# Kernel optimization log

Measured on AMD Instinct MI355X. Metric: run time of the kernel, lower is better.

Reference implementation:

```python
import jax, jax.numpy as jnp
import numpy as np
from jax.ops import segment_sum

N_NODES = 500_000
N_EDGES = 16_000_000


def gcn_conv(x, W, b, src, dst, n_nodes):
    """PyG GCNConv: linear transform, add self-loops, sym deg norm, scatter-add."""
    xw = x @ W  # [N, out]
    # degree including self-loop (edge weight 1 each)
    deg = segment_sum(jnp.ones((src.shape[0],), xw.dtype), dst, num_segments=n_nodes) + 1.0
    dinv = jax.lax.rsqrt(deg)  # deg^{-1/2}, deg >= 1 so safe
    norm = dinv[src] * dinv[dst]  # [E]
    msg = xw[src] * norm[:, None]  # [E, out]
    agg = segment_sum(msg, dst, num_segments=n_nodes)
    # self-loop contribution: norm_ii = dinv_i^2
    agg = agg + xw * (dinv * dinv)[:, None]
    return agg + b


def setup_inputs() -> dict:
    key = jax.random.key(0)
    ks = jax.random.split(key, 8)
    x = jax.random.normal(ks[0], (N_NODES, 2), dtype=jnp.float32)
    edge_index = jax.random.randint(ks[1], (2, N_EDGES), 0, N_NODES, dtype=jnp.int64)
    def glorot(k, fan_in, fan_out):
        s = jnp.sqrt(6.0 / (fan_in + fan_out))
        return jax.random.uniform(k, (fan_in, fan_out), jnp.float32, -s, s)
    return {
        "x": x,
        "edge_index": edge_index,
        "W1": glorot(ks[2], 2, 4), "b1": jnp.zeros((4,), jnp.float32),
        "W2": glorot(ks[3], 4, 4), "b2": jnp.zeros((4,), jnp.float32),
        "W3": glorot(ks[4], 4, 2), "b3": jnp.zeros((2,), jnp.float32),
    }


def reference(x, edge_index, W1, b1, W2, b2, W3, b3):
    src, dst = edge_index[0], edge_index[1]
    n = x.shape[0]
    h = jnp.tanh(gcn_conv(x, W1, b1, src, dst, n))
    h = jnp.tanh(gcn_conv(h, W2, b2, src, dst, n))
    h = gcn_conv(h, W3, b3, src, dst, n)
    return h
```

## Files before the change

kernel.cpp:

```cpp
#include <hip/hip_runtime.h>
#include <hip/hip_fp16.h>


#define TPB 256
#define T_TILE 16384
#define FBB 10
#define FB_MAX 512
#define CAP_F 34048
#define EB_CAP 34048

__global__ void initcur(int* __restrict__ cur, int FB) {
    int t = threadIdx.x;
    if (t < FB) cur[t] = t * CAP_F;
}

__global__ void __launch_bounds__(512)
scatter1(const int* __restrict__ dst, const int* __restrict__ src,
         int* __restrict__ cur, unsigned* __restrict__ pk1, int E, int FB) {
    __shared__ unsigned lpk[T_TILE];
    __shared__ int lhist[FB_MAX];
    __shared__ int lexcl[FB_MAX];
    __shared__ int lcur[FB_MAX];
    __shared__ int lbase[FB_MAX];
    int blk = blockIdx.x, tid = threadIdx.x;
    lhist[tid] = 0;
    __syncthreads();
    int base = blk * T_TILE;
    #pragma unroll 8
    for (int it = 0; it < T_TILE / 512; ++it) {
        int e = base + it * 512 + tid;
        if (e < E) atomicAdd(&lhist[((unsigned)dst[e]) >> FBB], 1);
    }
    __syncthreads();
    int hv = lhist[tid];
    lexcl[tid] = hv;
    __syncthreads();
    for (int off = 1; off < FB_MAX; off <<= 1) {
        int a = (tid >= off) ? lexcl[tid - off] : 0;
        __syncthreads();
        lexcl[tid] += a;
        __syncthreads();
    }
    lexcl[tid] -= hv;
    lcur[tid] = lexcl[tid];
    if (tid < FB && hv > 0) lbase[tid] = atomicAdd(&cur[tid], hv);
    __syncthreads();
    #pragma unroll 8
    for (int it = 0; it < T_TILE / 512; ++it) {
        int e = base + it * 512 + tid;
        if (e < E) {
            unsigned d = (unsigned)dst[e];
            unsigned s = (unsigned)src[e];
            int pos = atomicAdd(&lcur[d >> FBB], 1);
            lpk[pos] = (d & 1023u) | (s << FBB);
        }
    }
    __syncthreads();
    int w = tid >> 6, lane = tid & 63;
    for (int fb = w; fb < FB; fb += 8) {
        int cntb = lhist[fb];
        if (cntb == 0) continue;
        int lo = lexcl[fb], gb = lbase[fb];
        for (int t2 = lane; t2 < cntb; t2 += 64)
            pk1[gb + t2] = lpk[lo + t2];
    }
}

__global__ void bases_fix(const int* __restrict__ cur, int* __restrict__ csrbase,
                          int* __restrict__ rowptr, int FB, int N, int E) {
    __shared__ int lds[FB_MAX];
    int t = threadIdx.x;
    int c = (t < FB) ? (cur[t] - t * CAP_F) : 0;
    lds[t] = c;
    __syncthreads();
    for (int off = 1; off < FB_MAX; off <<= 1) {
        int a = (t >= off) ? lds[t - off] : 0;
        __syncthreads();
        lds[t] += a;
        __syncthreads();
    }
    if (t < FB) csrbase[t] = lds[t] - c;
    if (t == 0) { csrbase[FB] = E; rowptr[N] = E; }
}

__global__ void __launch_bounds__(1024)
buildfine(const unsigned* __restrict__ pk1, const int* __restrict__ csrbase,
          const float* __restrict__ x, int* __restrict__ rowptr,
          float* __restrict__ dinv, unsigned* __restrict__ z1h,
          unsigned* __restrict__ csr, int N) {
    __shared__ int cnt[1024];
    __shared__ int tmp[1024];
    __shared__ int cur[1024];
    __shared__ unsigned eb[EB_CAP];
    int fb = blockIdx.x, tid = threadIdx.x;
    int cb = csrbase[fb];
    int n = csrbase[fb + 1] - cb;
    size_t pbase = (size_t)fb * CAP_F;
    cnt[tid] = 0;
    __syncthreads();
    int k0 = 0;
    for (; k0 + 8192 <= n; k0 += 8192) {
        unsigned p[8];
        #pragma unroll
        for (int u = 0; u < 8; ++u) p[u] = pk1[pbase + k0 + tid + u * 1024];
        #pragma unroll
        for (int u = 0; u < 8; ++u) atomicAdd(&cnt[p[u] & 1023u], 1);
    }
    for (int k = k0 + tid; k < n; k += 1024)
        atomicAdd(&cnt[pk1[pbase + k] & 1023u], 1);
    __syncthreads();
    int c = cnt[tid];
    tmp[tid] = c;
    __syncthreads();
    for (int o = 1; o < 1024; o <<= 1) {
        int a = (tid >= o) ? tmp[tid - o] : 0;
        __syncthreads();
        tmp[tid] += a;
        __syncthreads();
    }
    int excl = tmp[tid] - c;
    int i = (fb << FBB) + tid;
    if (i < N) {
        rowptr[i] = cb + excl;
        float di = rsqrtf((float)c + 1.0f);
        dinv[i] = di;
        float2 xv = ((const float2*)x)[i];
        __half2 hz = __floats2half2_rn(xv.x * di, xv.y * di);
        z1h[i] = *(unsigned*)&hz;
    }
    cur[tid] = excl;
    __syncthreads();
    if (n <= EB_CAP) {
        k0 = 0;
        for (; k0 + 8192 <= n; k0 += 8192) {
            unsigned p[8];
            #pragma unroll
            for (int u = 0; u < 8; ++u) p[u] = pk1[pbase + k0 + tid + u * 1024];
            #pragma unroll
            for (int u = 0; u < 8; ++u) {
                int pos = atomicAdd(&cur[p[u] & 1023u], 1);
                eb[pos] = p[u] >> FBB;
            }
        }
        for (int k = k0 + tid; k < n; k += 1024) {
            unsigned p = pk1[pbase + k];
            int pos = atomicAdd(&cur[p & 1023u], 1);
            eb[pos] = p >> FBB;
        }
        __syncthreads();
        for (int k = tid; k < n; k += 1024) csr[cb + k] = eb[k];
    } else {
        for (int k = tid; k < n; k += 1024) {
            unsigned p = pk1[pbase + k];
            int pos = atomicAdd(&cur[p & 1023u], 1);
            csr[cb + pos] = p >> FBB;
        }
    }
}


__global__ void gcn1(const int* __restrict__ rowptr, const unsigned* __restrict__ csr,
                     const unsigned* __restrict__ z1h, const float* __restrict__ W1,
                     const float* __restrict__ b1, const float* __restrict__ dinv,
                     uint2* __restrict__ z2h, int N) {
    int i = blockIdx.x * blockDim.x + threadIdx.x;
    if (i >= N) return;
    int r0 = rowptr[i], r1 = rowptr[i + 1];
    float a0, a1;
    {
        unsigned zr = z1h[i];
        float2 zi = __half22float2(*(__half2*)&zr);
        a0 = zi.x; a1 = zi.y;
    }
    int k = r0;
    for (; k + 16 <= r1; k += 16) {
        unsigned j[16];
        #pragma unroll
        for (int u = 0; u < 16; ++u) j[u] = __builtin_nontemporal_load(&csr[k + u]);
        unsigned raw[16];
        #pragma unroll
        for (int u = 0; u < 16; ++u) raw[u] = z1h[j[u]];
        #pragma unroll
        for (int u = 0; u < 16; ++u) {
            float2 v = __half22float2(*(__half2*)&raw[u]);
            a0 += v.x; a1 += v.y;
        }
    }
    for (; k < r1; ++k) {
        unsigned zr = z1h[csr[k]];
        float2 zv = __half22float2(*(__half2*)&zr);
        a0 += zv.x; a1 += zv.y;
    }
    float di = dinv[i];
    float g0 = di * a0, g1 = di * a1;
    float o0 = di * tanhf(fmaf(g0, W1[0], fmaf(g1, W1[4], b1[0])));
    float o1 = di * tanhf(fmaf(g0, W1[1], fmaf(g1, W1[5], b1[1])));
    float o2 = di * tanhf(fmaf(g0, W1[2], fmaf(g1, W1[6], b1[2])));
    float o3 = di * tanhf(fmaf(g0, W1[3], fmaf(g1, W1[7], b1[3])));
    __half2 ha = __floats2half2_rn(o0, o1);
    __half2 hb = __floats2half2_rn(o2, o3);
    uint2 packed;
    packed.x = *(unsigned*)&ha;
    packed.y = *(unsigned*)&hb;
    z2h[i] = packed;
}

__global__ void gcn2(const int* __restrict__ rowptr, const unsigned* __restrict__ csr,
                     const uint2* __restrict__ z2h, const float* __restrict__ W2,
                     const float* __restrict__ b2, const float* __restrict__ W3,
                     const float* __restrict__ dinv, unsigned* __restrict__ z3h, int N) {
    int i = blockIdx.x * blockDim.x + threadIdx.x;
    if (i >= N) return;
    int r0 = rowptr[i], r1 = rowptr[i + 1];
    float a0, a1, a2, a3;
    {
        uint2 raw = z2h[i];
        float2 f01 = __half22float2(*(__half2*)&raw.x);
        float2 f23 = __half22float2(*(__half2*)&raw.y);
        a0 = f01.x; a1 = f01.y; a2 = f23.x; a3 = f23.y;
    }
    int k = r0;
    for (; k + 8 <= r1; k += 8) {
        unsigned j[8];
        #pragma unroll
        for (int u = 0; u < 8; ++u) j[u] = __builtin_nontemporal_load(&csr[k + u]);
        uint2 raw[8];
        #pragma unroll
        for (int u = 0; u < 8; ++u) raw[u] = z2h[j[u]];
        #pragma unroll
        for (int u = 0; u < 8; ++u) {
            float2 f01 = __half22float2(*(__half2*)&raw[u].x);
            float2 f23 = __half22float2(*(__half2*)&raw[u].y);
            a0 += f01.x; a1 += f01.y; a2 += f23.x; a3 += f23.y;
        }
    }
    for (; k < r1; ++k) {
        uint2 raw = z2h[csr[k]];
        float2 f01 = __half22float2(*(__half2*)&raw.x);
        float2 f23 = __half22float2(*(__half2*)&raw.y);
        a0 += f01.x; a1 += f01.y; a2 += f23.x; a3 += f23.y;
    }
    float di = dinv[i];
    float g0 = di * a0, g1 = di * a1, g2 = di * a2, g3 = di * a3;
    float h[4];
    #pragma unroll
    for (int c = 0; c < 4; ++c)
        h[c] = tanhf(b2[c] + g0 * W2[c] + g1 * W2[4 + c] + g2 * W2[8 + c] + g3 * W2[12 + c]);
    float v0 = h[0] * W3[0] + h[1] * W3[2] + h[2] * W3[4] + h[3] * W3[6];
    float v1 = h[0] * W3[1] + h[1] * W3[3] + h[2] * W3[5] + h[3] * W3[7];
    __half2 hz = __floats2half2_rn(v0 * di, v1 * di);
    z3h[i] = *(unsigned*)&hz;
}

__global__ void gcn3(const int* __restrict__ rowptr, const unsigned* __restrict__ csr,
                     const unsigned* __restrict__ z3h, const float* __restrict__ b3,
                     const float* __restrict__ dinv, float* __restrict__ out, int N) {
    int i = blockIdx.x * blockDim.x + threadIdx.x;
    if (i >= N) return;
    int r0 = rowptr[i], r1 = rowptr[i + 1];
    float a0, a1;
    {
        unsigned zr = z3h[i];
        float2 zi = __half22float2(*(__half2*)&zr);
        a0 = zi.x; a1 = zi.y;
    }
    int k = r0;
    for (; k + 16 <= r1; k += 16) {
        unsigned j[16];
        #pragma unroll
        for (int u = 0; u < 16; ++u) j[u] = __builtin_nontemporal_load(&csr[k + u]);
        unsigned raw[16];
        #pragma unroll
        for (int u = 0; u < 16; ++u) raw[u] = z3h[j[u]];
        #pragma unroll
        for (int u = 0; u < 16; ++u) {
            float2 v = __half22float2(*(__half2*)&raw[u]);
            a0 += v.x; a1 += v.y;
        }
    }
    for (; k < r1; ++k) {
        unsigned zr = z3h[csr[k]];
        float2 zv = __half22float2(*(__half2*)&zr);
        a0 += zv.x; a1 += zv.y;
    }
    float di = dinv[i];
    ((float2*)out)[i] = make_float2(fmaf(di, a0, b3[0]), fmaf(di, a1, b3[1]));
}

extern "C" void kernel_launch(void* const* d_in, const int* in_sizes, int n_in,
                              void* d_out, int out_size, void* d_ws, size_t ws_size,
                              hipStream_t stream) {
    const float* x  = (const float*)d_in[0];
    const int*   ei = (const int*)d_in[1];
    const float* W1 = (const float*)d_in[2];
    const float* b1 = (const float*)d_in[3];
    const float* W2 = (const float*)d_in[4];
    const float* b2 = (const float*)d_in[5];
    const float* W3 = (const float*)d_in[6];
    const float* b3 = (const float*)d_in[7];
    float* out = (float*)d_out;

    const int N = in_sizes[0] / 2;
    const int E = in_sizes[1] / 2;
    const int* src = ei;
    const int* dst = ei + E;

    const int FB  = (N + (1 << FBB) - 1) >> FBB;
    const int ntB = (E + T_TILE - 1) / T_TILE;

    auto align = [](size_t o) { return (o + 255) & ~(size_t)255; };
    char* wbase = (char*)d_ws;
    size_t off = 0;
    float*    dinv    = (float*)(wbase + off);    off = align(off + (size_t)N * 4);
    unsigned* z1h     = (unsigned*)(wbase + off); off = align(off + (size_t)N * 4);
    uint2*    z2h     = (uint2*)(wbase + off);    off = align(off + (size_t)N * 8);
    unsigned* z3h     = (unsigned*)(wbase + off); off = align(off + (size_t)N * 4);
    int*      rowptr  = (int*)(wbase + off);      off = align(off + (size_t)(N + 1) * 4);
    int*      cur     = (int*)(wbase + off);      off = align(off + (size_t)FB_MAX * 4);
    int*      csrbase = (int*)(wbase + off);      off = align(off + (size_t)(FB_MAX + 1) * 4);
    unsigned* pk1     = (unsigned*)(wbase + off); off = align(off + (size_t)FB * CAP_F * 4);
    unsigned* csr     = (unsigned*)(wbase + off); off = align(off + (size_t)E * 4);

    dim3 gN((N + TPB - 1) / TPB);
    initcur<<<dim3(1), dim3(512), 0, stream>>>(cur, FB);
    scatter1<<<dim3(ntB), dim3(512), 0, stream>>>(dst, src, cur, pk1, E, FB);
    bases_fix<<<dim3(1), dim3(512), 0, stream>>>(cur, csrbase, rowptr, FB, N, E);
    buildfine<<<dim3(FB), dim3(1024), 0, stream>>>(pk1, csrbase, x, rowptr, dinv,
                                                   z1h, csr, N);
    gcn1<<<gN, dim3(TPB), 0, stream>>>(rowptr, csr, z1h, W1, b1, dinv, z2h, N);
    gcn2<<<gN, dim3(TPB), 0, stream>>>(rowptr, csr, z2h, W2, b2, W3, dinv, z3h, N);
    gcn3<<<gN, dim3(TPB), 0, stream>>>(rowptr, csr, z3h, b3, dinv, out, N);
}
```

Measured before the change: 715.4 us.

## Drop CSR build; aggregate per dst bucket with LDS atomics from packed edges

Replaces the fine CSR construction (prefix scan, local sort, CSR write) with a degree-only pass. Each layer now walks the coarse dst-bucketed packed edge array per 1024-node block and accumulates neighbour features with shared-memory float atomics. This removes one full pass that writes the CSR and the rowptr indirection. In exchange, every layer pays LDS atomics per edge, only FB (~489) blocks run, and the summation order becomes nondeterministic.

New measurement: 988.5 us. +38.2%, slower.

```diff
diff --git a/kernel.cpp b/kernel.cpp
--- a/kernel.cpp
+++ b/kernel.cpp
@@ -7,7 +7,6 @@
 #define FBB 10
 #define FB_MAX 512
 #define CAP_F 34048
-#define EB_CAP 34048
 
 __global__ void initcur(int* __restrict__ cur, int FB) {
     int t = threadIdx.x;
@@ -66,225 +65,261 @@
     }
 }
 
-__global__ void bases_fix(const int* __restrict__ cur, int* __restrict__ csrbase,
-                          int* __restrict__ rowptr, int FB, int N, int E) {
-    __shared__ int lds[FB_MAX];
-    int t = threadIdx.x;
-    int c = (t < FB) ? (cur[t] - t * CAP_F) : 0;
-    lds[t] = c;
-    __syncthreads();
-    for (int off = 1; off < FB_MAX; off <<= 1) {
-        int a = (t >= off) ? lds[t - off] : 0;
-        __syncthreads();
-        lds[t] += a;
-        __syncthreads();
-    }
-    if (t < FB) csrbase[t] = lds[t] - c;
-    if (t == 0) { csrbase[FB] = E; rowptr[N] = E; }
-}
-
 __global__ void __launch_bounds__(1024)
-buildfine(const unsigned* __restrict__ pk1, const int* __restrict__ csrbase,
-          const float* __restrict__ x, int* __restrict__ rowptr,
-          float* __restrict__ dinv, unsigned* __restrict__ z1h,
-          unsigned* __restrict__ csr, int N) {
-    __shared__ int cnt[1024];
-    __shared__ int tmp[1024];
-    __shared__ int cur[1024];
-    __shared__ unsigned eb[EB_CAP];
+builddeg(const unsigned* __restrict__ pk1, const int* __restrict__ cur,
+         const float* __restrict__ x, float* __restrict__ dinv,
+         unsigned* __restrict__ z1h, int N) {
+    __shared__ int deg[1024];
     int fb = blockIdx.x, tid = threadIdx.x;
-    int cb = csrbase[fb];
-    int n = csrbase[fb + 1] - cb;
+    deg[tid] = 0;
+    __syncthreads();
     size_t pbase = (size_t)fb * CAP_F;
-    cnt[tid] = 0;
-    __syncthreads();
+    int n = cur[fb] - (int)(fb * CAP_F);
     int k0 = 0;
     for (; k0 + 8192 <= n; k0 += 8192) {
         unsigned p[8];
         #pragma unroll
-        for (int u = 0; u < 8; ++u) p[u] = pk1[pbase + k0 + tid + u * 1024];
-        #pragma unroll
-        for (int u = 0; u < 8; ++u) atomicAdd(&cnt[p[u] & 1023u], 1);
+        for (int u = 0; u < 8; ++u)
+            p[u] = __builtin_nontemporal_load(&pk1[pbase + k0 + tid + u * 1024]);
+        #pragma unroll
+        for (int u = 0; u < 8; ++u) atomicAdd(&deg[p[u] & 1023u], 1);
     }
     for (int k = k0 + tid; k < n; k += 1024)
-        atomicAdd(&cnt[pk1[pbase + k] & 1023u], 1);
-    __syncthreads();
-    int c = cnt[tid];
-    tmp[tid] = c;
-    __syncthreads();
-    for (int o = 1; o < 1024; o <<= 1) {
-        int a = (tid >= o) ? tmp[tid - o] : 0;
-        __syncthreads();
-        tmp[tid] += a;
-        __syncthreads();
-    }
-    int excl = tmp[tid] - c;
+        atomicAdd(&deg[__builtin_nontemporal_load(&pk1[pbase + k]) & 1023u], 1);
+    __syncthreads();
     int i = (fb << FBB) + tid;
     if (i < N) {
-        rowptr[i] = cb + excl;
-        float di = rsqrtf((float)c + 1.0f);
+        float di = rsqrtf((float)deg[tid] + 1.0f);
         dinv[i] = di;
         float2 xv = ((const float2*)x)[i];
         __half2 hz = __floats2half2_rn(xv.x * di, xv.y * di);
         z1h[i] = *(unsigned*)&hz;
     }
-    cur[tid] = excl;
-    __syncthreads();
-    if (n <= EB_CAP) {
-        k0 = 0;
-        for (; k0 + 8192 <= n; k0 += 8192) {
-            unsigned p[8];
-            #pragma unroll
-            for (int u = 0; u < 8; ++u) p[u] = pk1[pbase + k0 + tid + u * 1024];
-            #pragma unroll
-            for (int u = 0; u < 8; ++u) {
-                int pos = atomicAdd(&cur[p[u] & 1023u], 1);
-                eb[pos] = p[u] >> FBB;
-            }
-        }
-        for (int k = k0 + tid; k < n; k += 1024) {
-            unsigned p = pk1[pbase + k];
-            int pos = atomicAdd(&cur[p & 1023u], 1);
-            eb[pos] = p >> FBB;
-        }
-        __syncthreads();
-        for (int k = tid; k < n; k += 1024) csr[cb + k] = eb[k];
-    } else {
-        for (int k = tid; k < n; k += 1024) {
-            unsigned p = pk1[pbase + k];
-            int pos = atomicAdd(&cur[p & 1023u], 1);
-            csr[cb + pos] = p >> FBB;
-        }
-    }
-}
-
-
-__global__ void gcn1(const int* __restrict__ rowptr, const unsigned* __restrict__ csr,
-                     const unsigned* __restrict__ z1h, const float* __restrict__ W1,
-                     const float* __restrict__ b1, const float* __restrict__ dinv,
-                     uint2* __restrict__ z2h, int N) {
-    int i = blockIdx.x * blockDim.x + threadIdx.x;
-    if (i >= N) return;
-    int r0 = rowptr[i], r1 = rowptr[i + 1];
-    float a0, a1;
-    {
+}
+
+
+__global__ void __launch_bounds__(1024)
+glayer1(const unsigned* __restrict__ pk1, const int* __restrict__ cur,
+        const unsigned* __restrict__ z1h, const float* __restrict__ dinv,
+        const float* __restrict__ W1, const float* __restrict__ b1,
+        uint2* __restrict__ z2h, int N) {
+    __shared__ float acc[2048];
+    int fb = blockIdx.x, tid = threadIdx.x;
+    acc[tid] = 0.f; acc[tid + 1024] = 0.f;
+    __syncthreads();
+    size_t pbase = (size_t)fb * CAP_F;
+    int n = cur[fb] - (int)(fb * CAP_F);
+    int k0 = 0;
+    for (; k0 + 16384 <= n; k0 += 16384) {
+        unsigned p[16];
+        #pragma unroll
+        for (int u = 0; u < 16; ++u)
+            p[u] = __builtin_nontemporal_load(&pk1[pbase + k0 + tid + u * 1024]);
+        unsigned raw[16];
+        #pragma unroll
+        for (int u = 0; u < 16; ++u) raw[u] = z1h[p[u] >> FBB];
+        #pragma unroll
+        for (int u = 0; u < 16; ++u) {
+            float2 v = __half22float2(*(__half2*)&raw[u]);
+            unsigned d = (p[u] & 1023u) << 1;
+            atomicAdd(&acc[d], v.x);
+            atomicAdd(&acc[d + 1], v.y);
+        }
+    }
+    for (; k0 + 4096 <= n; k0 += 4096) {
+        unsigned p[4];
+        #pragma unroll
+        for (int u = 0; u < 4; ++u)
+            p[u] = __builtin_nontemporal_load(&pk1[pbase + k0 + tid + u * 1024]);
+        unsigned raw[4];
+        #pragma unroll
+        for (int u = 0; u < 4; ++u) raw[u] = z1h[p[u] >> FBB];
+        #pragma unroll
+        for (int u = 0; u < 4; ++u) {
+            float2 v = __half22float2(*(__half2*)&raw[u]);
+            unsigned d = (p[u] & 1023u) << 1;
+            atomicAdd(&acc[d], v.x);
+            atomicAdd(&acc[d + 1], v.y);
+        }
+    }
+    for (int k = k0 + tid; k < n; k += 1024) {
+        unsigned p = __builtin_nontemporal_load(&pk1[pbase + k]);
+        unsigned zr = z1h[p >> FBB];
+        float2 v = __half22float2(*(__half2*)&zr);
+        unsigned d = (p & 1023u) << 1;
+        atomicAdd(&acc[d], v.x);
+        atomicAdd(&acc[d + 1], v.y);
+    }
+    __syncthreads();
+    int i = (fb << FBB) + tid;
+    if (i < N) {
         unsigned zr = z1h[i];
         float2 zi = __half22float2(*(__half2*)&zr);
-        a0 = zi.x; a1 = zi.y;
-    }
-    int k = r0;
-    for (; k + 16 <= r1; k += 16) {
-        unsigned j[16];
-        #pragma unroll
-        for (int u = 0; u < 16; ++u) j[u] = __builtin_nontemporal_load(&csr[k + u]);
+        float di = dinv[i];
+        float g0 = di * (acc[tid * 2] + zi.x);
+        float g1 = di * (acc[tid * 2 + 1] + zi.y);
+        float o0 = di * tanhf(fmaf(g0, W1[0], fmaf(g1, W1[4], b1[0])));
+        float o1 = di * tanhf(fmaf(g0, W1[1], fmaf(g1, W1[5], b1[1])));
+        float o2 = di * tanhf(fmaf(g0, W1[2], fmaf(g1, W1[6], b1[2])));
+        float o3 = di * tanhf(fmaf(g0, W1[3], fmaf(g1, W1[7], b1[3])));
+        __half2 ha = __floats2half2_rn(o0, o1);
+        __half2 hb = __floats2half2_rn(o2, o3);
+        uint2 packed;
+        packed.x = *(unsigned*)&ha;
+        packed.y = *(unsigned*)&hb;
+        z2h[i] = packed;
+    }
+}
+
+__global__ void __launch_bounds__(1024)
+glayer2(const unsigned* __restrict__ pk1, const int* __restrict__ cur,
+        const unsigned long long* __restrict__ z2h, const float* __restrict__ dinv,
+        const float* __restrict__ W2, const float* __restrict__ b2,
+        const float* __restrict__ W3, unsigned* __restrict__ z3h, int N) {
+    __shared__ float acc[4096];
+    int fb = blockIdx.x, tid = threadIdx.x;
+    #pragma unroll
+    for (int u = 0; u < 4; ++u) acc[tid + u * 1024] = 0.f;
+    __syncthreads();
+    size_t pbase = (size_t)fb * CAP_F;
+    int n = cur[fb] - (int)(fb * CAP_F);
+    int k0 = 0;
+    for (; k0 + 8192 <= n; k0 += 8192) {
+        unsigned p[8];
+        #pragma unroll
+        for (int u = 0; u < 8; ++u)
+            p[u] = __builtin_nontemporal_load(&pk1[pbase + k0 + tid + u * 1024]);
+        unsigned long long raw[8];
+        #pragma unroll
+        for (int u = 0; u < 8; ++u) raw[u] = z2h[p[u] >> FBB];
+        #pragma unroll
+        for (int u = 0; u < 8; ++u) {
+            unsigned lo = (unsigned)raw[u], hi = (unsigned)(raw[u] >> 32);
+            float2 f01 = __half22float2(*(__half2*)&lo);
+            float2 f23 = __half22float2(*(__half2*)&hi);
+            unsigned d = (p[u] & 1023u) << 2;
+            atomicAdd(&acc[d], f01.x);
+            atomicAdd(&acc[d + 1], f01.y);
+            atomicAdd(&acc[d + 2], f23.x);
+            atomicAdd(&acc[d + 3], f23.y);
+        }
+    }
+    for (; k0 + 4096 <= n; k0 += 4096) {
+        unsigned p[4];
+        #pragma unroll
+        for (int u = 0; u < 4; ++u)
+            p[u] = __builtin_nontemporal_load(&pk1[pbase + k0 + tid + u * 1024]);
+        unsigned long long raw[4];
+        #pragma unroll
+        for (int u = 0; u < 4; ++u) raw[u] = z2h[p[u] >> FBB];
+        #pragma unroll
+        for (int u = 0; u < 4; ++u) {
+            unsigned lo = (unsigned)raw[u], hi = (unsigned)(raw[u] >> 32);
+            float2 f01 = __half22float2(*(__half2*)&lo);
+            float2 f23 = __half22float2(*(__half2*)&hi);
+            unsigned d = (p[u] & 1023u) << 2;
+            atomicAdd(&acc[d], f01.x);
+            atomicAdd(&acc[d + 1], f01.y);
+            atomicAdd(&acc[d + 2], f23.x);
+            atomicAdd(&acc[d + 3], f23.y);
+        }
+    }
+    for (int k = k0 + tid; k < n; k += 1024) {
+        unsigned p = __builtin_nontemporal_load(&pk1[pbase + k]);
+        unsigned long long zr = z2h[p >> FBB];
+        unsigned lo = (unsigned)zr, hi = (unsigned)(zr >> 32);
+        float2 f01 = __half22float2(*(__half2*)&lo);
+        float2 f23 = __half22float2(*(__half2*)&hi);
+        unsigned d = (p & 1023u) << 2;
+        atomicAdd(&acc[d], f01.x);
+        atomicAdd(&acc[d + 1], f01.y);
+        atomicAdd(&acc[d + 2], f23.x);
+        atomicAdd(&acc[d + 3], f23.y);
+    }
+    __syncthreads();
+    int i = (fb << FBB) + tid;
+    if (i < N) {
+        unsigned long long zr = z2h[i];
+        unsigned lo = (unsigned)zr, hi = (unsigned)(zr >> 32);
+        float2 f01 = __half22float2(*(__half2*)&lo);
+        float2 f23 = __half22float2(*(__half2*)&hi);
+        float di = dinv[i];
+        float g0 = di * (acc[tid * 4] + f01.x);
+        float g1 = di * (acc[tid * 4 + 1] + f01.y);
+        float g2 = di * (acc[tid * 4 + 2] + f23.x);
+        float g3 = di * (acc[tid * 4 + 3] + f23.y);
+        float h[4];
+        #pragma unroll
+        for (int c = 0; c < 4; ++c)
+            h[c] = tanhf(b2[c] + g0 * W2[c] + g1 * W2[4 + c] + g2 * W2[8 + c] + g3 * W2[12 + c]);
+        float v0 = h[0] * W3[0] + h[1] * W3[2] + h[2] * W3[4] + h[3] * W3[6];
+        float v1 = h[0] * W3[1] + h[1] * W3[3] + h[2] * W3[5] + h[3] * W3[7];
+        __half2 hz = __floats2half2_rn(v0 * di, v1 * di);
+        z3h[i] = *(unsigned*)&hz;
+    }
+}
+
+__global__ void __launch_bounds__(1024)
+glayer3(const unsigned* __restrict__ pk1, const int* __restrict__ cur,
+        const unsigned* __restrict__ z3h, const float* __restrict__ dinv,
+        const float* __restrict__ b3, float* __restrict__ out, int N) {
+    __shared__ float acc[2048];
+    int fb = blockIdx.x, tid = threadIdx.x;
+    acc[tid] = 0.f; acc[tid + 1024] = 0.f;
+    __syncthreads();
+    size_t pbase = (size_t)fb * CAP_F;
+    int n = cur[fb] - (int)(fb * CAP_F);
+    int k0 = 0;
+    for (; k0 + 16384 <= n; k0 += 16384) {
+        unsigned p[16];
+        #pragma unroll
+        for (int u = 0; u < 16; ++u)
+            p[u] = __builtin_nontemporal_load(&pk1[pbase + k0 + tid + u * 1024]);
         unsigned raw[16];
         #pragma unroll
-        for (int u = 0; u < 16; ++u) raw[u] = z1h[j[u]];
+        for (int u = 0; u < 16; ++u) raw[u] = z3h[p[u] >> FBB];
         #pragma unroll
         for (int u = 0; u < 16; ++u) {
             float2 v = __half22float2(*(__half2*)&raw[u]);
-            a0 += v.x; a1 += v.y;
-        }
-    }
-    for (; k < r1; ++k) {
-        unsigned zr = z1h[csr[k]];
-        float2 zv = __half22float2(*(__half2*)&zr);
-        a0 += zv.x; a1 += zv.y;
-    }
-    float di = dinv[i];
-    float g0 = di * a0, g1 = di * a1;
-    float o0 = di * tanhf(fmaf(g0, W1[0], fmaf(g1, W1[4], b1[0])));
-    float o1 = di * tanhf(fmaf(g0, W1[1], fmaf(g1, W1[5], b1[1])));
-    float o2 = di * tanhf(fmaf(g0, W1[2], fmaf(g1, W1[6], b1[2])));
-    float o3 = di * tanhf(fmaf(g0, W1[3], fmaf(g1, W1[7], b1[3])));
-    __half2 ha = __floats2half2_rn(o0, o1);
-    __half2 hb = __floats2half2_rn(o2, o3);
-    uint2 packed;
-    packed.x = *(unsigned*)&ha;
-    packed.y = *(unsigned*)&hb;
-    z2h[i] = packed;
-}
-
-__global__ void gcn2(const int* __restrict__ rowptr, const unsigned* __restrict__ csr,
-                     const uint2* __restrict__ z2h, const float* __restrict__ W2,
-                     const float* __restrict__ b2, const float* __restrict__ W3,
-                     const float* __restrict__ dinv, unsigned* __restrict__ z3h, int N) {
-    int i = blockIdx.x * blockDim.x + threadIdx.x;
-    if (i >= N) return;
-    int r0 = rowptr[i], r1 = rowptr[i + 1];
-    float a0, a1, a2, a3;
-    {
-        uint2 raw = z2h[i];
-        float2 f01 = __half22float2(*(__half2*)&raw.x);
-        float2 f23 = __half22float2(*(__half2*)&raw.y);
-        a0 = f01.x; a1 = f01.y; a2 = f23.x; a3 = f23.y;
-    }
-    int k = r0;
-    for (; k + 8 <= r1; k += 8) {
-        unsigned j[8];
-        #pragma unroll
-        for (int u = 0; u < 8; ++u) j[u] = __builtin_nontemporal_load(&csr[k + u]);
-        uint2 raw[8];
-        #pragma unroll
-        for (int u = 0; u < 8; ++u) raw[u] = z2h[j[u]];
-        #pragma unroll
-        for (int u = 0; u < 8; ++u) {
-            float2 f01 = __half22float2(*(__half2*)&raw[u].x);
-            float2 f23 = __half22float2(*(__half2*)&raw[u].y);
-            a0 += f01.x; a1 += f01.y; a2 += f23.x; a3 += f23.y;
-        }
-    }
-    for (; k < r1; ++k) {
-        uint2 raw = z2h[csr[k]];
-        float2 f01 = __half22float2(*(__half2*)&raw.x);
-        float2 f23 = __half22float2(*(__half2*)&raw.y);
-        a0 += f01.x; a1 += f01.y; a2 += f23.x; a3 += f23.y;
-    }
-    float di = dinv[i];
-    float g0 = di * a0, g1 = di * a1, g2 = di * a2, g3 = di * a3;
-    float h[4];
-    #pragma unroll
-    for (int c = 0; c < 4; ++c)
-        h[c] = tanhf(b2[c] + g0 * W2[c] + g1 * W2[4 + c] + g2 * W2[8 + c] + g3 * W2[12 + c]);
-    float v0 = h[0] * W3[0] + h[1] * W3[2] + h[2] * W3[4] + h[3] * W3[6];
-    float v1 = h[0] * W3[1] + h[1] * W3[3] + h[2] * W3[5] + h[3] * W3[7];
-    __half2 hz = __floats2half2_rn(v0 * di, v1 * di);
-    z3h[i] = *(unsigned*)&hz;
-}
-
-__global__ void gcn3(const int* __restrict__ rowptr, const unsigned* __restrict__ csr,
-                     const unsigned* __restrict__ z3h, const float* __restrict__ b3,
-                     const float* __restrict__ dinv, float* __restrict__ out, int N) {
-    int i = blockIdx.x * blockDim.x + threadIdx.x;
-    if (i >= N) return;
-    int r0 = rowptr[i], r1 = rowptr[i + 1];
-    float a0, a1;
-    {
+            unsigned d = (p[u] & 1023u) << 1;
+            atomicAdd(&acc[d], v.x);
+            atomicAdd(&acc[d + 1], v.y);
+        }
+    }
+    for (; k0 + 4096 <= n; k0 += 4096) {
+        unsigned p[4];
+        #pragma unroll
+        for (int u = 0; u < 4; ++u)
+            p[u] = __builtin_nontemporal_load(&pk1[pbase + k0 + tid + u * 1024]);
+        unsigned raw[4];
+        #pragma unroll
+        for (int u = 0; u < 4; ++u) raw[u] = z3h[p[u] >> FBB];
+        #pragma unroll
+        for (int u = 0; u < 4; ++u) {
+            float2 v = __half22float2(*(__half2*)&raw[u]);
+            unsigned d = (p[u] & 1023u) << 1;
+            atomicAdd(&acc[d], v.x);
+            atomicAdd(&acc[d + 1], v.y);
+        }
+    }
+    for (int k = k0 + tid; k < n; k += 1024) {
+        unsigned p = __builtin_nontemporal_load(&pk1[pbase + k]);
+        unsigned zr = z3h[p >> FBB];
+        float2 v = __half22float2(*(__half2*)&zr);
+        unsigned d = (p & 1023u) << 1;
+        atomicAdd(&acc[d], v.x);
+        atomicAdd(&acc[d + 1], v.y);
+    }
+    __syncthreads();
+    int i = (fb << FBB) + tid;
+    if (i < N) {
         unsigned zr = z3h[i];
         float2 zi = __half22float2(*(__half2*)&zr);
-        a0 = zi.x; a1 = zi.y;
-    }
-    int k = r0;
-    for (; k + 16 <= r1; k += 16) {
-        unsigned j[16];
-        #pragma unroll
-        for (int u = 0; u < 16; ++u) j[u] = __builtin_nontemporal_load(&csr[k + u]);
-        unsigned raw[16];
-        #pragma unroll
-        for (int u = 0; u < 16; ++u) raw[u] = z3h[j[u]];
-        #pragma unroll
-        for (int u = 0; u < 16; ++u) {
-            float2 v = __half22float2(*(__half2*)&raw[u]);
-            a0 += v.x; a1 += v.y;
-        }
-    }
-    for (; k < r1; ++k) {
-        unsigned zr = z3h[csr[k]];
-        float2 zv = __half22float2(*(__half2*)&zr);
-        a0 += zv.x; a1 += zv.y;
-    }
-    float di = dinv[i];
-    ((float2*)out)[i] = make_float2(fmaf(di, a0, b3[0]), fmaf(di, a1, b3[1]));
+        float di = dinv[i];
+        float a0 = acc[tid * 2] + zi.x;
+        float a1 = acc[tid * 2 + 1] + zi.y;
+        ((float2*)out)[i] = make_float2(fmaf(di, a0, b3[0]), fmaf(di, a1, b3[1]));
+    }
 }
 
 extern "C" void kernel_launch(void* const* d_in, const int* in_sizes, int n_in,
@@ -311,23 +346,20 @@
     auto align = [](size_t o) { return (o + 255) & ~(size_t)255; };
     char* wbase = (char*)d_ws;
     size_t off = 0;
-    float*    dinv    = (float*)(wbase + off);    off = align(off + (size_t)N * 4);
-    unsigned* z1h     = (unsigned*)(wbase + off); off = align(off + (size_t)N * 4);
-    uint2*    z2h     = (uint2*)(wbase + off);    off = align(off + (size_t)N * 8);
-    unsigned* z3h     = (unsigned*)(wbase + off); off = align(off + (size_t)N * 4);
-    int*      rowptr  = (int*)(wbase + off);      off = align(off + (size_t)(N + 1) * 4);
-    int*      cur     = (int*)(wbase + off);      off = align(off + (size_t)FB_MAX * 4);
-    int*      csrbase = (int*)(wbase + off);      off = align(off + (size_t)(FB_MAX + 1) * 4);
-    unsigned* pk1     = (unsigned*)(wbase + off); off = align(off + (size_t)FB * CAP_F * 4);
-    unsigned* csr     = (unsigned*)(wbase + off); off = align(off + (size_t)E * 4);
-
-    dim3 gN((N + TPB - 1) / TPB);
+    float*    dinv = (float*)(wbase + off);    off = align(off + (size_t)N * 4);
+    unsigned* z1h  = (unsigned*)(wbase + off); off = align(off + (size_t)N * 4);
+    unsigned long long* z2h = (unsigned long long*)(wbase + off);
+    off = align(off + (size_t)N * 8);
+    unsigned* z3h  = (unsigned*)(wbase + off); off = align(off + (size_t)N * 4);
+    int*      cur  = (int*)(wbase + off);      off = align(off + (size_t)FB_MAX * 4);
+    unsigned* pk1  = (unsigned*)(wbase + off); off = align(off + (size_t)FB * CAP_F * 4);
+
     initcur<<<dim3(1), dim3(512), 0, stream>>>(cur, FB);
     scatter1<<<dim3(ntB), dim3(512), 0, stream>>>(dst, src, cur, pk1, E, FB);
-    bases_fix<<<dim3(1), dim3(512), 0, stream>>>(cur, csrbase, rowptr, FB, N, E);
-    buildfine<<<dim3(FB), dim3(1024), 0, stream>>>(pk1, csrbase, x, rowptr, dinv,
-                                                   z1h, csr, N);
-    gcn1<<<gN, dim3(TPB), 0, stream>>>(rowptr, csr, z1h, W1, b1, dinv, z2h, N);
-    gcn2<<<gN, dim3(TPB), 0, stream>>>(rowptr, csr, z2h, W2, b2, W3, dinv, z3h, N);
-    gcn3<<<gN, dim3(TPB), 0, stream>>>(rowptr, csr, z3h, b3, dinv, out, N);
-}
+    builddeg<<<dim3(FB), dim3(1024), 0, stream>>>(pk1, cur, x, dinv, z1h, N);
+    glayer1<<<dim3(FB), dim3(1024), 0, stream>>>(pk1, cur, z1h, dinv, W1, b1,
+                                                 (uint2*)z2h, N);
+    glayer2<<<dim3(FB), dim3(1024), 0, stream>>>(pk1, cur, z2h, dinv, W2, b2, W3,
+                                                 z3h, N);
+    glayer3<<<dim3(FB), dim3(1024), 0, stream>>>(pk1, cur, z3h, dinv, b3, out, N);
+}
```

## Sort nodes by degree within blocks to balance per-thread gather work

Applied to the files above, without the earlier changes.

Builds a per-1024-node-block permutation that groups nodes by in-degree (capped at 127) using a small shared histogram and scan in buildfine. The three GCN layer kernels then process nodes in permuted order, so threads in a wavefront have similar edge counts and less divergence in the gather loop. gcn2's gather unroll also grows from 8 to 16. The cost is an extra perm read per thread, less coalesced rowptr/dinv/output accesses, and more register pressure in gcn2.

Measured after the change: 850.4 us. 18.9% more time.

```diff
diff --git a/kernel.cpp b/kernel.cpp
--- a/kernel.cpp
+++ b/kernel.cpp
@@ -87,16 +87,19 @@
 buildfine(const unsigned* __restrict__ pk1, const int* __restrict__ csrbase,
           const float* __restrict__ x, int* __restrict__ rowptr,
           float* __restrict__ dinv, unsigned* __restrict__ z1h,
-          unsigned* __restrict__ csr, int N) {
+          unsigned* __restrict__ csr, int* __restrict__ perm, int N) {
     __shared__ int cnt[1024];
     __shared__ int tmp[1024];
     __shared__ int cur[1024];
     __shared__ unsigned eb[EB_CAP];
+    __shared__ int dh[128];
+    __shared__ int dcur[128];
     int fb = blockIdx.x, tid = threadIdx.x;
     int cb = csrbase[fb];
     int n = csrbase[fb + 1] - cb;
     size_t pbase = (size_t)fb * CAP_F;
     cnt[tid] = 0;
+    if (tid < 128) dh[tid] = 0;
     __syncthreads();
     int k0 = 0;
     for (; k0 + 8192 <= n; k0 += 8192) {
@@ -129,6 +132,23 @@
         z1h[i] = *(unsigned*)&hz;
     }
     cur[tid] = excl;
+    int dcap = (c < 127) ? c : 127;
+    if (i < N) atomicAdd(&dh[dcap], 1);
+    __syncthreads();
+    if (tid < 128) dcur[tid] = dh[tid];
+    __syncthreads();
+    for (int o = 1; o < 128; o <<= 1) {
+        int a = (tid < 128 && tid >= o) ? dcur[tid - o] : 0;
+        __syncthreads();
+        if (tid < 128) dcur[tid] += a;
+        __syncthreads();
+    }
+    if (tid < 128) dcur[tid] -= dh[tid];
+    __syncthreads();
+    if (i < N) {
+        int r = atomicAdd(&dcur[dcap], 1);
+        perm[(fb << FBB) + r] = i;
+    }
     __syncthreads();
     if (n <= EB_CAP) {
         k0 = 0;
@@ -160,11 +180,13 @@
 
 
 __global__ void gcn1(const int* __restrict__ rowptr, const unsigned* __restrict__ csr,
+                     const int* __restrict__ perm,
                      const unsigned* __restrict__ z1h, const float* __restrict__ W1,
                      const float* __restrict__ b1, const float* __restrict__ dinv,
                      uint2* __restrict__ z2h, int N) {
-    int i = blockIdx.x * blockDim.x + threadIdx.x;
-    if (i >= N) return;
+    int ii = blockIdx.x * blockDim.x + threadIdx.x;
+    if (ii >= N) return;
+    int i = perm[ii];
     int r0 = rowptr[i], r1 = rowptr[i + 1];
     float a0, a1;
     {
@@ -206,11 +228,13 @@
 }
 
 __global__ void gcn2(const int* __restrict__ rowptr, const unsigned* __restrict__ csr,
+                     const int* __restrict__ perm,
                      const uint2* __restrict__ z2h, const float* __restrict__ W2,
                      const float* __restrict__ b2, const float* __restrict__ W3,
                      const float* __restrict__ dinv, unsigned* __restrict__ z3h, int N) {
-    int i = blockIdx.x * blockDim.x + threadIdx.x;
-    if (i >= N) return;
+    int ii = blockIdx.x * blockDim.x + threadIdx.x;
+    if (ii >= N) return;
+    int i = perm[ii];
     int r0 = rowptr[i], r1 = rowptr[i + 1];
     float a0, a1, a2, a3;
     {
@@ -220,15 +244,15 @@
         a0 = f01.x; a1 = f01.y; a2 = f23.x; a3 = f23.y;
     }
     int k = r0;
-    for (; k + 8 <= r1; k += 8) {
-        unsigned j[8];
-        #pragma unroll
-        for (int u = 0; u < 8; ++u) j[u] = __builtin_nontemporal_load(&csr[k + u]);
-        uint2 raw[8];
-        #pragma unroll
-        for (int u = 0; u < 8; ++u) raw[u] = z2h[j[u]];
-        #pragma unroll
-        for (int u = 0; u < 8; ++u) {
+    for (; k + 16 <= r1; k += 16) {
+        unsigned j[16];
+        #pragma unroll
+        for (int u = 0; u < 16; ++u) j[u] = __builtin_nontemporal_load(&csr[k + u]);
+        uint2 raw[16];
+        #pragma unroll
+        for (int u = 0; u < 16; ++u) raw[u] = z2h[j[u]];
+        #pragma unroll
+        for (int u = 0; u < 16; ++u) {
             float2 f01 = __half22float2(*(__half2*)&raw[u].x);
             float2 f23 = __half22float2(*(__half2*)&raw[u].y);
             a0 += f01.x; a1 += f01.y; a2 += f23.x; a3 += f23.y;
@@ -253,10 +277,12 @@
 }
 
 __global__ void gcn3(const int* __restrict__ rowptr, const unsigned* __restrict__ csr,
+                     const int* __restrict__ perm,
                      const unsigned* __restrict__ z3h, const float* __restrict__ b3,
                      const float* __restrict__ dinv, float* __restrict__ out, int N) {
-    int i = blockIdx.x * blockDim.x + threadIdx.x;
-    if (i >= N) return;
+    int ii = blockIdx.x * blockDim.x + threadIdx.x;
+    if (ii >= N) return;
+    int i = perm[ii];
     int r0 = rowptr[i], r1 = rowptr[i + 1];
     float a0, a1;
     {
@@ -316,6 +342,7 @@
     uint2*    z2h     = (uint2*)(wbase + off);    off = align(off + (size_t)N * 8);
     unsigned* z3h     = (unsigned*)(wbase + off); off = align(off + (size_t)N * 4);
     int*      rowptr  = (int*)(wbase + off);      off = align(off + (size_t)(N + 1) * 4);
+    int*      perm    = (int*)(wbase + off);      off = align(off + (size_t)N * 4);
     int*      cur     = (int*)(wbase + off);      off = align(off + (size_t)FB_MAX * 4);
     int*      csrbase = (int*)(wbase + off);      off = align(off + (size_t)(FB_MAX + 1) * 4);
     unsigned* pk1     = (unsigned*)(wbase + off); off = align(off + (size_t)FB * CAP_F * 4);
@@ -326,8 +353,8 @@
     scatter1<<<dim3(ntB), dim3(512), 0, stream>>>(dst, src, cur, pk1, E, FB);
     bases_fix<<<dim3(1), dim3(512), 0, stream>>>(cur, csrbase, rowptr, FB, N, E);
     buildfine<<<dim3(FB), dim3(1024), 0, stream>>>(pk1, csrbase, x, rowptr, dinv,
-                                                   z1h, csr, N);
-    gcn1<<<gN, dim3(TPB), 0, stream>>>(rowptr, csr, z1h, W1, b1, dinv, z2h, N);
-    gcn2<<<gN, dim3(TPB), 0, stream>>>(rowptr, csr, z2h, W2, b2, W3, dinv, z3h, N);
-    gcn3<<<gN, dim3(TPB), 0, stream>>>(rowptr, csr, z3h, b3, dinv, out, N);
-}
+                                                   z1h, csr, perm, N);
+    gcn1<<<gN, dim3(TPB), 0, stream>>>(rowptr, csr, perm, z1h, W1, b1, dinv, z2h, N);
+    gcn2<<<gN, dim3(TPB), 0, stream>>>(rowptr, csr, perm, z2h, W2, b2, W3, dinv, z3h, N);
+    gcn3<<<gN, dim3(TPB), 0, stream>>>(rowptr, csr, perm, z3h, b3, dinv, out, N);
+}
```

## Double scatter tile, use wavefront shuffle scans, flush bucketed edges by binary search

Applied to the files above, without the earlier changes.

The scatter kernel's edge tile grows from 16384 to 32768, so each block reserves global bucket space with fewer atomics. The LDS Hillis-Steele prefix scans in scatter1 and buildfine become two-level wavefront __shfl_up scans, removing many block-wide barriers. The scatter flush loop changes from one wave per bucket to one thread per element, finding each element's bucket by binary search over the bucket offsets, which keeps writes balanced. The larger tile needs more LDS per block and may lower occupancy, and the binary search adds per-element LDS reads.

Result: slower. 816.1 us (+14.1%).

```diff
diff --git a/kernel.cpp b/kernel.cpp
--- a/kernel.cpp
+++ b/kernel.cpp
@@ -3,7 +3,7 @@
 
 
 #define TPB 256
-#define T_TILE 16384
+#define T_TILE 32768
 #define FBB 10
 #define FB_MAX 512
 #define CAP_F 34048
@@ -22,10 +22,13 @@
     __shared__ int lexcl[FB_MAX];
     __shared__ int lcur[FB_MAX];
     __shared__ int lbase[FB_MAX];
+    __shared__ int wsum[8];
     int blk = blockIdx.x, tid = threadIdx.x;
+    int lane = tid & 63, w = tid >> 6;
     lhist[tid] = 0;
     __syncthreads();
     int base = blk * T_TILE;
+    int ntile = (E - base < T_TILE) ? (E - base) : T_TILE;
     #pragma unroll 8
     for (int it = 0; it < T_TILE / 512; ++it) {
         int e = base + it * 512 + tid;
@@ -33,16 +36,27 @@
     }
     __syncthreads();
     int hv = lhist[tid];
-    lexcl[tid] = hv;
-    __syncthreads();
-    for (int off = 1; off < FB_MAX; off <<= 1) {
-        int a = (tid >= off) ? lexcl[tid - off] : 0;
-        __syncthreads();
-        lexcl[tid] += a;
-        __syncthreads();
-    }
-    lexcl[tid] -= hv;
-    lcur[tid] = lexcl[tid];
+    int sv = hv;
+    #pragma unroll
+    for (int d = 1; d < 64; d <<= 1) {
+        int sy = __shfl_up(sv, d, 64);
+        if (lane >= d) sv += sy;
+    }
+    if (lane == 63) wsum[w] = sv;
+    __syncthreads();
+    if (tid < 64) {
+        int s = (tid < 8) ? wsum[tid] : 0;
+        #pragma unroll
+        for (int d = 1; d < 8; d <<= 1) {
+            int sy = __shfl_up(s, d, 64);
+            if (tid >= d) s += sy;
+        }
+        if (tid < 8) wsum[tid] = s;
+    }
+    __syncthreads();
+    int excl = ((w > 0) ? wsum[w - 1] : 0) + sv - hv;
+    lexcl[tid] = excl;
+    lcur[tid] = excl;
     if (tid < FB && hv > 0) lbase[tid] = atomicAdd(&cur[tid], hv);
     __syncthreads();
     #pragma unroll 8
@@ -56,13 +70,13 @@
         }
     }
     __syncthreads();
-    int w = tid >> 6, lane = tid & 63;
-    for (int fb = w; fb < FB; fb += 8) {
-        int cntb = lhist[fb];
-        if (cntb == 0) continue;
-        int lo = lexcl[fb], gb = lbase[fb];
-        for (int t2 = lane; t2 < cntb; t2 += 64)
-            pk1[gb + t2] = lpk[lo + t2];
+    for (int k = tid; k < ntile; k += 512) {
+        int lo = 0, hi = FB - 1;
+        while (lo < hi) {
+            int mid = (lo + hi + 1) >> 1;
+            if (lexcl[mid] <= k) lo = mid; else hi = mid - 1;
+        }
+        pk1[lbase[lo] + (k - lexcl[lo])] = lpk[k];
     }
 }
 
@@ -89,10 +103,11 @@
           float* __restrict__ dinv, unsigned* __restrict__ z1h,
           unsigned* __restrict__ csr, int N) {
     __shared__ int cnt[1024];
-    __shared__ int tmp[1024];
     __shared__ int cur[1024];
     __shared__ unsigned eb[EB_CAP];
+    __shared__ int wsum[16];
     int fb = blockIdx.x, tid = threadIdx.x;
+    int lane = tid & 63, w = tid >> 6;
     int cb = csrbase[fb];
     int n = csrbase[fb + 1] - cb;
     size_t pbase = (size_t)fb * CAP_F;
@@ -110,15 +125,25 @@
         atomicAdd(&cnt[pk1[pbase + k] & 1023u], 1);
     __syncthreads();
     int c = cnt[tid];
-    tmp[tid] = c;
-    __syncthreads();
-    for (int o = 1; o < 1024; o <<= 1) {
-        int a = (tid >= o) ? tmp[tid - o] : 0;
-        __syncthreads();
-        tmp[tid] += a;
-        __syncthreads();
-    }
-    int excl = tmp[tid] - c;
+    int sv = c;
+    #pragma unroll
+    for (int d = 1; d < 64; d <<= 1) {
+        int sy = __shfl_up(sv, d, 64);
+        if (lane >= d) sv += sy;
+    }
+    if (lane == 63) wsum[w] = sv;
+    __syncthreads();
+    if (tid < 64) {
+        int s = (tid < 16) ? wsum[tid] : 0;
+        #pragma unroll
+        for (int d = 1; d < 16; d <<= 1) {
+            int sy = __shfl_up(s, d, 64);
+            if (tid >= d) s += sy;
+        }
+        if (tid < 16) wsum[tid] = s;
+    }
+    __syncthreads();
+    int excl = ((w > 0) ? wsum[w - 1] : 0) + sv - c;
     int i = (fb << FBB) + tid;
     if (i < N) {
         rowptr[i] = cb + excl;
```
